# Optimization experiments

Measured on AMD Instinct MI355X. Metric: run time of the kernel, lower is better.

The kernel has to match this reference:

```python
import jax, jax.numpy as jnp
import numpy as np

SHAPE = (4, 16, 16)          # (t, h, w) latent shape
E, H, L = 576, 16, 6         # embd_dim, n_head, n_layer
DK = E // H                  # head dim = 36
SEQ = int(np.prod(SHAPE))    # 1024
B = 2


def _layernorm(x, s, b):
    m = x.mean(-1, keepdims=True)
    v = ((x - m) ** 2).mean(-1, keepdims=True)
    return (x - m) * jax.lax.rsqrt(v + 1e-5) * s + b


def _masks():
    # causal lower-triangular mask and L1 distance-decay mask (FullAttention.__init__)
    causal = np.tril(np.ones((SEQ, SEQ), dtype=bool))
    grids = np.meshgrid(*[np.arange(s) for s in SHAPE], indexing='ij')
    coords = np.stack([g.ravel() for g in grids], -1)          # [SEQ, 3]
    dist = np.abs(coords[:, None, :] - coords[None, :, :]).sum(-1).astype(np.float32)
    dm = np.exp(-dist / dist[0, -1])                            # max distance = dist[0, SEQ-1]
    return jnp.asarray(causal), jnp.asarray(dm)


def setup_inputs() -> dict:
    key = jax.random.key(0)
    ks = jax.random.split(key, 12)
    f32 = jnp.float32
    std = 1.0 / np.sqrt(E)
    pe = E // 3
    d = {}
    d['x'] = jax.random.normal(ks[0], (B, *SHAPE, E), f32)
    d['sos'] = jax.random.normal(ks[1], (E,), f32) * 0.02
    d['pe0'] = jax.random.normal(ks[2], (SHAPE[0], pe), f32) * 0.01
    d['pe1'] = jax.random.normal(ks[3], (SHAPE[1], pe), f32) * 0.01
    d['pe2'] = jax.random.normal(ks[4], (SHAPE[2], pe), f32) * 0.01
    d['ln1_s'] = jnp.ones((L, E), f32); d['ln1_b'] = jnp.zeros((L, E), f32)
    d['wq'] = jax.random.normal(ks[5], (L, E, E), f32) * std
    d['wk'] = jax.random.normal(ks[6], (L, E, E), f32) * std
    d['wv'] = jax.random.normal(ks[7], (L, E, E), f32) * std
    d['wo'] = jax.random.normal(ks[8], (L, E, E), f32) * (1.0 / np.sqrt(E * L))
    d['bo'] = jnp.zeros((L, E), f32)
    d['ln2_s'] = jnp.ones((L, E), f32); d['ln2_b'] = jnp.zeros((L, E), f32)
    d['w1'] = jax.random.normal(ks[9], (L, E, 4 * E), f32) * std
    d['b1'] = jnp.zeros((L, 4 * E), f32)
    d['w2'] = jax.random.normal(ks[10], (L, 4 * E, E), f32) * (1.0 / np.sqrt(4 * E))
    d['b2'] = jnp.zeros((L, E), f32)
    return d


def _forward(x, sos, pe0, pe1, pe2, ln1_s, ln1_b, wq, wk, wv, wo, bo,
             ln2_s, ln2_b, w1, b1, w2, b2):
    b = x.shape[0]
    causal, dm = _masks()
    h = x.reshape(b, SEQ, E)
    # RightShift: prepend learned SOS token, drop last
    h = jnp.concatenate([jnp.broadcast_to(sos, (b, 1, E)), h[:, :-1]], axis=1)
    # AddBroadcastPosEmbed (dim=-1): per-axis embeddings concatenated on channels
    pos = jnp.concatenate([
        jnp.broadcast_to(pe0[:, None, None, :], (*SHAPE, E // 3)),
        jnp.broadcast_to(pe1[None, :, None, :], (*SHAPE, E // 3)),
        jnp.broadcast_to(pe2[None, None, :, :], (*SHAPE, E // 3)),
    ], axis=-1).reshape(SEQ, E)
    h = h + pos
    scale = 1.0 / np.sqrt(DK)
    for l in range(L):  # fixed small layer loop
        y = _layernorm(h, ln1_s[l], ln1_b[l])
        q = (y @ wq[l]).reshape(b, SEQ, H, DK).transpose(0, 2, 1, 3)
        k = (y @ wk[l]).reshape(b, SEQ, H, DK).transpose(0, 2, 1, 3)
        v = (y @ wv[l]).reshape(b, SEQ, H, DK).transpose(0, 2, 1, 3)
        s = jnp.einsum('bhqd,bhkd->bhqk', q, k) * scale
        s = s * dm                              # elementwise distance-decay mask
        s = jnp.where(causal, s, -jnp.inf)       # causal masked_fill
        a = jax.nn.softmax(s, axis=-1)
        o = jnp.einsum('bhqk,bhkd->bhqd', a, v)
        o = o.transpose(0, 2, 1, 3).reshape(b, SEQ, E) @ wo[l] + bo[l]
        h = h + o
        y = _layernorm(h, ln2_s[l], ln2_b[l])
        y1 = y @ w1[l] + b1[l]
        y1 = jax.nn.sigmoid(1.702 * y1) * y1     # GeLU2
        h = h + (y1 @ w2[l] + b2[l])
    return h.reshape(b, *SHAPE, E)


def reference(x, sos, pe0, pe1, pe2, ln1_s, ln1_b, wq, wk, wv, wo, bo,
              ln2_s, ln2_b, w1, b1, w2, b2):
    return _forward(x, sos, pe0, pe1, pe2, ln1_s, ln1_b, wq, wk, wv, wo, bo,
                    ln2_s, ln2_b, w1, b1, w2, b2)
```

## Files before the change

kernel.cpp:

```cpp
#include <hip/hip_runtime.h>


#define E_    576
#define SEQ_  1024
#define B_    2
#define NH_   16
#define DK_   36
#define DKP_  64
#define NL_   6
#define FF_   2304
#define ROWS_ 2048
#define PSTRIDE_ 1179648

typedef unsigned short u16;
typedef unsigned int u32;
typedef float f32x4 __attribute__((ext_vector_type(4)));
typedef float f32x16 __attribute__((ext_vector_type(16)));
typedef __bf16 bf16x8 __attribute__((ext_vector_type(8)));
typedef __bf16 bf16x4 __attribute__((ext_vector_type(4)));

#define MFMA16(a, b, c) __builtin_amdgcn_mfma_f32_16x16x32_bf16((a), (b), (c), 0, 0, 0)
#define MFMA32(a, b, c) __builtin_amdgcn_mfma_f32_32x32x16_bf16((a), (b), (c), 0, 0, 0)

__device__ __forceinline__ float bf2f(u16 u) {
    return __uint_as_float(((unsigned)u) << 16);
}
__device__ __forceinline__ u16 f2bf(float f) {
    unsigned u = __float_as_uint(f);
    u += 0x7fffu + ((u >> 16) & 1u);
    return (u16)(u >> 16);
}
__device__ __forceinline__ float load_in(const void* p, size_t i, int isf32) {
    return isf32 ? ((const float*)p)[i] : bf2f(((const u16*)p)[i]);
}
__device__ __forceinline__ bf16x8 ldg8(const u16* p) {
    uint4 u = *(const uint4*)p;
    bf16x8 r;
    __builtin_memcpy(&r, &u, 16);
    return r;
}
__device__ __forceinline__ void gload_lds16(const u16* g, u16* l) {
    __builtin_amdgcn_global_load_lds(
        (const __attribute__((address_space(1))) unsigned int*)g,
        (__attribute__((address_space(3))) unsigned int*)l, 16, 0, 0);
}

__global__ void detect_kernel(const u16* __restrict__ x, int* __restrict__ flag)
{
    __shared__ float red[4];
    int lane = threadIdx.x & 63, wave = threadIdx.x >> 6;
    float mx = 0.f;
    for (int i = threadIdx.x; i < 4096; i += 256) {
        float v = fabsf(bf2f(x[i]));
        if (v < 3e38f) mx = fmaxf(mx, v);
    }
    for (int off = 1; off < 64; off <<= 1) mx = fmaxf(mx, __shfl_xor(mx, off));
    if (lane == 0) red[wave] = mx;
    __syncthreads();
    if (threadIdx.x == 0) {
        float m = fmaxf(fmaxf(red[0], red[1]), fmaxf(red[2], red[3]));
        *flag = (m > 1e6f) ? 1 : 0;
    }
}

__global__ __launch_bounds__(256) void repack_kernel(
    const void* __restrict__ wq, const void* __restrict__ wk,
    const void* __restrict__ wv, const void* __restrict__ wo,
    const void* __restrict__ w1, const void* __restrict__ w2,
    u16* __restrict__ wT, const int* __restrict__ flagp)
{
    __shared__ u32 tile[64 * 33];
    int isf32 = *flagp;
    int idx = blockIdx.x, l = blockIdx.z;
    const void* src;
    u16* dst;
    size_t sbase;
    int R, C, cx, ry;
    if (idx < 324) {
        int t4 = idx / 81, rem = idx - t4 * 81;
        ry = rem / 9; cx = rem % 9; R = 576; C = 576;
        src = (t4 == 0) ? wq : (t4 == 1) ? wk : (t4 == 2) ? wv : wo;
        sbase = (size_t)l * 331776;
        dst = wT + (size_t)l * 3981312 + t4 * 331776;
    } else if (idx < 648) {
        int rem = idx - 324;
        ry = rem / 36; cx = rem % 36; R = 576; C = 2304;
        src = w1; sbase = (size_t)l * 1327104;
        dst = wT + (size_t)l * 3981312 + 1327104;
    } else {
        int rem = idx - 648;
        ry = rem / 9; cx = rem % 9; R = 2304; C = 576;
        src = w2; sbase = (size_t)l * 1327104;
        dst = wT + (size_t)l * 3981312 + 2654208;
    }
    int r0 = ry * 64, c0 = cx * 64;
    int t = threadIdx.x;
    if (isf32) {
        int chunk = t & 15, row = t >> 4;
        f32x4 vf4[4];
        #pragma unroll
        for (int i = 0; i < 4; i++) {
            int rr = row + i * 16;
            size_t g = sbase + (size_t)(r0 + rr) * C + c0 + chunk * 4;
            vf4[i] = *(const f32x4*)((const float*)src + g);
        }
        #pragma unroll
        for (int i = 0; i < 4; i++) {
            int rr = row + i * 16;
            u32 lo = (u32)f2bf(vf4[i][0]) | ((u32)f2bf(vf4[i][1]) << 16);
            u32 hi = (u32)f2bf(vf4[i][2]) | ((u32)f2bf(vf4[i][3]) << 16);
            tile[rr * 33 + chunk * 2] = lo;
            tile[rr * 33 + chunk * 2 + 1] = hi;
        }
    } else {
        int c8 = t & 7, row = t >> 3;
        uint4 vq[2];
        #pragma unroll
        for (int i = 0; i < 2; i++) {
            int rr = row + i * 32;
            size_t g = sbase + (size_t)(r0 + rr) * C + c0 + c8 * 8;
            vq[i] = *(const uint4*)((const u16*)src + g);
        }
        #pragma unroll
        for (int i = 0; i < 2; i++) {
            int rr = row + i * 32;
            u32* w = &tile[rr * 33 + c8 * 4];
            w[0] = vq[i].x; w[1] = vq[i].y; w[2] = vq[i].z; w[3] = vq[i].w;
        }
    }
    __syncthreads();
    u16* tbase = dst + ((size_t)cx * (R >> 6) + ry) * 4096;
    int k8 = t & 7, nl = t >> 3;
    #pragma unroll
    for (int i = 0; i < 2; i++) {
        int nn = nl + i * 32;
        int hw = nn >> 1, sh = (nn & 1) * 16;
        u32 v[8];
        #pragma unroll
        for (int j = 0; j < 8; j++)
            v[j] = (tile[(8 * k8 + j) * 33 + hw] >> sh) & 0xffffu;
        uint4 o;
        o.x = v[0] | (v[1] << 16);
        o.y = v[2] | (v[3] << 16);
        o.z = v[4] | (v[5] << 16);
        o.w = v[6] | (v[7] << 16);
        ((uint4*)(tbase + nn * 64))[k8 ^ (nn & 7)] = o;
    }
}

__global__ void embed_kernel(
    const void* __restrict__ x, const void* __restrict__ sos,
    const void* __restrict__ pe0, const void* __restrict__ pe1,
    const void* __restrict__ pe2, float* __restrict__ h,
    const int* __restrict__ flagp)
{
    int isf32 = *flagp;
    int row = blockIdx.x;
    int e = threadIdx.x;
    int s = row & 1023;
    float v = (s == 0) ? load_in(sos, e, isf32)
                       : load_in(x, (size_t)(row - 1) * E_ + e, isf32);
    int t = s >> 8, hh = (s >> 4) & 15, ww = s & 15;
    float p = (e < 192) ? load_in(pe0, t * 192 + e, isf32)
            : (e < 384) ? load_in(pe1, hh * 192 + e - 192, isf32)
                        : load_in(pe2, ww * 192 + e - 384, isf32);
    h[(size_t)row * E_ + e] = v + p;
}

template <int NPART>
__global__ __launch_bounds__(256) void ln_kernel(
    float* __restrict__ h, u16* __restrict__ y,
    const float* __restrict__ parts,
    const void* __restrict__ sc, const void* __restrict__ bi,
    int off0, const int* __restrict__ flagp)
{
    int isf32 = *flagp;
    int lane = threadIdx.x & 63, wave = threadIdx.x >> 6;
    int row = blockIdx.x * 4 + wave;
    float* hr = h + (size_t)row * E_;
    float v[9], s = 0.f, sq = 0.f;
    #pragma unroll
    for (int j = 0; j < 9; j++) {
        int e = lane + j * 64;
        float t = hr[e];
        #pragma unroll
        for (int pk = 0; pk < NPART; pk++)
            t += parts[(size_t)pk * PSTRIDE_ + (size_t)row * E_ + e];
        if (NPART > 0) hr[e] = t;
        v[j] = t;
        s += t;
        sq += t * t;
    }
    for (int off = 1; off < 64; off <<= 1) {
        s += __shfl_xor(s, off);
        sq += __shfl_xor(sq, off);
    }
    float mean = s * (1.0f / E_);
    float var = sq * (1.0f / E_) - mean * mean;
    float r = rsqrtf(var + 1e-5f);
    #pragma unroll
    for (int j = 0; j < 9; j++) {
        int e = lane + j * 64;
        float sce = load_in(sc, off0 + e, isf32);
        float bie = load_in(bi, off0 + e, isf32);
        y[(size_t)row * E_ + e] = f2bf((v[j] - mean) * r * sce + bie);
    }
}

template <int MODE, int SPLITK>
__global__ __launch_bounds__(512) void gemm_kernel(
    const u16* __restrict__ A, const u16* __restrict__ BtBase, int K,
    const void* __restrict__ bias, int boff, float* __restrict__ pout,
    u16* __restrict__ out, u16* __restrict__ qb, u16* __restrict__ kb,
    u16* __restrict__ vtb, const int* __restrict__ flagp)
{
    __shared__ u16 lA[8192];
    __shared__ u16 lB[4096];
    int t = threadIdx.x;
    int lane = t & 63, wave = t >> 6;
    int lw = lane & 15, lq = lane >> 4;
    int wx = wave >> 1, wy = wave & 1;
    int m0 = blockIdx.x * 128, n0 = blockIdx.y * 64;
    int z = blockIdx.z / SPLITK, kz = blockIdx.z % SPLITK;
    int Ks = K / SPLITK, kbase = kz * Ks;

    const u16* Bt = BtBase + (MODE == 0 ? (size_t)z * 331776 : 0);
    int rowS = t >> 3;
    int gc = (t & 7) ^ (rowS & 7);
    const u16* gA = A + (size_t)(m0 + rowS) * K + kbase + gc * 8;
    const u16* gB = Bt + ((size_t)(n0 >> 6)) * ((size_t)K << 6)
                  + (size_t)kbase * 64 + (size_t)t * 8;
    size_t rstep = (size_t)64 * K;

    f32x4 acc[2][2];
    for (int mi = 0; mi < 2; mi++)
        for (int ni = 0; ni < 2; ni++)
            for (int r = 0; r < 4; r++) acc[mi][ni][r] = 0.f;

    for (int kc = 0; kc < Ks; kc += 64) {
        gload_lds16(gA + kc,         &lA[t * 8]);
        gload_lds16(gA + rstep + kc, &lA[4096 + t * 8]);
        gload_lds16(gB + kc * 64,    &lB[t * 8]);
        __syncthreads();
        #pragma unroll
        for (int ks = 0; ks < 2; ks++) {
            int csw = ((ks * 4 + lq) ^ (lw & 7)) * 8;
            bf16x8 bf0 = ldg8(&lB[(wy * 32 + lw) * 64 + csw]);
            bf16x8 bf1 = ldg8(&lB[(wy * 32 + 16 + lw) * 64 + csw]);
            #pragma unroll
            for (int mi = 0; mi < 2; mi++) {
                bf16x8 af = ldg8(&lA[(wx * 32 + mi * 16 + lw) * 64 + csw]);
                acc[mi][0] = MFMA16(af, bf0, acc[mi][0]);
                acc[mi][1] = MFMA16(af, bf1, acc[mi][1]);
            }
        }
        __syncthreads();
    }

    int isf32 = (MODE != 0) ? *flagp : 0;
    #pragma unroll
    for (int ni = 0; ni < 2; ni++) {
        int n = n0 + wy * 32 + ni * 16 + lw;
        float bn = 0.f;
        if (MODE == 2 || ((MODE == 1 || MODE == 3) && kz == 0))
            bn = load_in(bias, boff + n, isf32);
        #pragma unroll
        for (int mi = 0; mi < 2; mi++) {
            #pragma unroll
            for (int r = 0; r < 4; r++) {
                int m = m0 + wx * 32 + mi * 16 + lq * 4 + r;
                float v = acc[mi][ni][r];
                if (MODE == 0) {
                    int b = m >> 10, s = m & 1023;
                    int head = n / 36, d = n - head * 36;
                    size_t bh = (size_t)(b * NH_ + head);
                    if (z == 0)
                        qb[(bh * SEQ_ + s) * DKP_ + d] = f2bf(v * (1.0f / 6.0f));
                    else if (z == 1)
                        kb[(bh * SEQ_ + s) * DKP_ + d] = f2bf(v);
                    else
                        vtb[(bh * DKP_ + d) * SEQ_ + s] = f2bf(v);
                } else if (MODE == 2) {
                    float tt = v + bn;
                    out[(size_t)m * FF_ + n] = f2bf(tt / (1.0f + __expf(-1.702f * tt)));
                } else {
                    pout[(size_t)kz * PSTRIDE_ + (size_t)m * E_ + n] = v + bn;
                }
            }
        }
    }
}

__global__ __launch_bounds__(256, 2) void attn_kernel(
    const u16* __restrict__ qb, const u16* __restrict__ kb,
    const u16* __restrict__ vtb, u16* __restrict__ ob)
{
    __shared__ float sm[4][32], sl[4][32], so[4][32][37];
    int lane = threadIdx.x & 63, wave = threadIdx.x >> 6;
    int q5 = lane & 31, hi = lane >> 5, hi8 = hi * 8;
    int L = blockIdx.x;
    int bh = L & 31;
    int qt = 31 - (L >> 5);
    int head = bh & 15, b = bh >> 4;
    int q0 = qt * 32;

    const u16* qrow = qb + ((size_t)bh * SEQ_ + q0 + q5) * DKP_ + hi8;
    bf16x8 qf[4];
    #pragma unroll
    for (int d16 = 0; d16 < 4; d16++) qf[d16] = ldg8(qrow + d16 * 16);

    int tq = q0 >> 8;
    int hq = ((q0 >> 4) & 15) + (q5 >> 4);
    int qg = q0 + q5;
    int wq = q5 & 15;
    float ew8[8];
    #pragma unroll
    for (int j = 0; j < 8; j++)
        ew8[j] = __expf((float)abs(wq - (j + hi8)) * (-1.0f / 33.0f));

    float m_i = -1e30f, l_i = 0.f;
    f32x16 oacc[2];
    #pragma unroll
    for (int Dt = 0; Dt < 2; Dt++)
        #pragma unroll
        for (int r = 0; r < 16; r++) oacc[Dt][r] = 0.f;

    int kp = (q5 & ~12) | ((q5 & 4) << 1) | ((q5 & 8) >> 1);
    const u16* kbh = kb + (size_t)bh * SEQ_ * DKP_;
    const u16* vbh = vtb + (size_t)bh * DKP_ * SEQ_;

    int nch = (qt >> 1) + 1;
    for (int c = wave; c < nch; c += 4) {
        int kv0 = c * 64;
        bf16x8 kf[2][4], vf[2][4];
        #pragma unroll
        for (int T = 0; T < 2; T++) {
            const u16* kr = kbh + (size_t)(kv0 + T * 32 + kp) * DKP_ + hi8;
            #pragma unroll
            for (int d16 = 0; d16 < 4; d16++) kf[T][d16] = ldg8(kr + d16 * 16);
        }
        #pragma unroll
        for (int s = 0; s < 4; s++)
            vf[0][s] = ldg8(vbh + (size_t)q5 * SEQ_ + kv0 + s * 16 + hi8);
        f32x16 st[2];
        #pragma unroll
        for (int T = 0; T < 2; T++) {
            f32x16 tt;
            #pragma unroll
            for (int r = 0; r < 16; r++) tt[r] = 0.f;
            #pragma unroll
            for (int d16 = 0; d16 < 4; d16++)
                tt = MFMA32(kf[T][d16], qf[d16], tt);
            st[T] = tt;
        }
        #pragma unroll
        for (int s = 0; s < 4; s++)
            vf[1][s] = ldg8(vbh + (size_t)(32 + q5) * SEQ_ + kv0 + s * 16 + hi8);
        int tk = kv0 >> 8, hk0 = (kv0 >> 4) & 15;
        float sB[4];
        #pragma unroll
        for (int i = 0; i < 4; i++)
            sB[i] = __expf((float)(abs(tq - tk) + abs(hq - hk0 - i))
                           * (-1.0f / 33.0f));
        float vv[2][16];
        #pragma unroll
        for (int T = 0; T < 2; T++)
            #pragma unroll
            for (int r = 0; r < 16; r++) {
                int j = (r & 3) + ((r >> 2) & 1) * 4;
                int hidx = T * 2 + ((r >> 3) & 1);
                vv[T][r] = st[T][r] * (sB[hidx] * ew8[j]);
            }
        if (c == nch - 1) {
            #pragma unroll
            for (int T = 0; T < 2; T++)
                #pragma unroll
                for (int r = 0; r < 16; r++) {
                    int key = kv0 + T * 32 + ((r >> 3) & 1) * 16 + hi8
                            + (r & 3) + ((r >> 2) & 1) * 4;
                    if (key > qg) vv[T][r] = -1e30f;
                }
        }
        float mloc = -1e30f;
        #pragma unroll
        for (int T = 0; T < 2; T++)
            #pragma unroll
            for (int r = 0; r < 16; r++) mloc = fmaxf(mloc, vv[T][r]);
        mloc = fmaxf(mloc, __shfl_xor(mloc, 32));
        float mn = fmaxf(m_i, mloc);
        float alpha = __expf(m_i - mn);
        m_i = mn;
        float p[2][16];
        float rs = 0.f;
        #pragma unroll
        for (int T = 0; T < 2; T++)
            #pragma unroll
            for (int r = 0; r < 16; r++) {
                p[T][r] = __expf(vv[T][r] - mn);
                rs += p[T][r];
            }
        rs += __shfl_xor(rs, 32);
        l_i = l_i * alpha + rs;
        #pragma unroll
        for (int Dt = 0; Dt < 2; Dt++)
            #pragma unroll
            for (int r = 0; r < 16; r++) oacc[Dt][r] *= alpha;
        bf16x8 pf[4];
        #pragma unroll
        for (int T = 0; T < 2; T++)
            #pragma unroll
            for (int sp = 0; sp < 2; sp++)
                #pragma unroll
                for (int e = 0; e < 8; e++)
                    pf[T * 2 + sp][e] = (__bf16)p[T][sp * 8 + e];
        #pragma unroll
        for (int Dt = 0; Dt < 2; Dt++)
            #pragma unroll
            for (int s = 0; s < 4; s++)
                oacc[Dt] = MFMA32(vf[Dt][s], pf[s], oacc[Dt]);
    }

    if (hi == 0) { sm[wave][q5] = m_i; sl[wave][q5] = l_i; }
    #pragma unroll
    for (int r = 0; r < 16; r++)
        so[wave][q5][(r & 3) + 8 * (r >> 2) + 4 * hi] = oacc[0][r];
    if (hi == 0) {
        #pragma unroll
        for (int r = 0; r < 4; r++)
            so[wave][q5][32 + r] = oacc[1][r];
    }
    __syncthreads();
    for (int i = threadIdx.x; i < 32 * DK_; i += 256) {
        int row = i / DK_, col = i - row * DK_;
        float M = fmaxf(fmaxf(sm[0][row], sm[1][row]),
                        fmaxf(sm[2][row], sm[3][row]));
        float Lm = 0.f, O = 0.f;
        #pragma unroll
        for (int w = 0; w < 4; w++) {
            float f = __expf(sm[w][row] - M);
            Lm += f * sl[w][row];
            O += f * so[w][row][col];
        }
        ob[((size_t)b * SEQ_ + q0 + row) * E_ + head * DK_ + col] = f2bf(O / Lm);
    }
}

__global__ void out_kernel(const float* __restrict__ h,
                           const float* __restrict__ p3,
                           void* __restrict__ out,
                           const int* __restrict__ flagp)
{
    int isf32 = *flagp;
    size_t i = (size_t)blockIdx.x * blockDim.x + threadIdx.x;
    float v = h[i] + p3[i] + p3[i + PSTRIDE_] + p3[i + 2 * PSTRIDE_]
            + p3[i + 3 * PSTRIDE_];
    if (isf32) ((float*)out)[i] = v;
    else       ((u16*)out)[i] = f2bf(v);
}

extern "C" void kernel_launch(void* const* d_in, const int* in_sizes, int n_in,
                              void* d_out, int out_size, void* d_ws,
                              size_t ws_size, hipStream_t stream)
{
    const void* x    = d_in[0];
    const void* sos  = d_in[1];
    const void* pe0  = d_in[2];
    const void* pe1  = d_in[3];
    const void* pe2  = d_in[4];
    const void* ln1s = d_in[5];
    const void* ln1b = d_in[6];
    const void* wq   = d_in[7];
    const void* wk   = d_in[8];
    const void* wv   = d_in[9];
    const void* wo   = d_in[10];
    const void* bo   = d_in[11];
    const void* ln2s = d_in[12];
    const void* ln2b = d_in[13];
    const void* w1   = d_in[14];
    const void* b1   = d_in[15];
    const void* w2   = d_in[16];
    const void* b2   = d_in[17];

    char* ws = (char*)d_ws;
    u16*   qbuf  = (u16*)(ws + 0);
    u16*   kbuf  = (u16*)(ws + 4194304);
    u16*   vtbuf = (u16*)(ws + 8388608);
    float* h     = (float*)(ws + 12582912);
    u16*   y     = (u16*)(ws + 17301504);
    u16*   o     = (u16*)(ws + 19660800);
    u16*   y1    = (u16*)(ws + 22020096);
    u16*   wT    = (u16*)(ws + 31457280);
    int*   flag  = (int*)(ws + 79233024);
    float* p1    = (float*)(ws + 83886080);
    float* p3    = (float*)(ws + 100663296);

    hipMemsetAsync(ws, 0, 12582912, stream);
    detect_kernel<<<1, 256, 0, stream>>>((const u16*)x, flag);
    repack_kernel<<<dim3(972, 1, 6), 256, 0, stream>>>(
        wq, wk, wv, wo, w1, w2, wT, flag);
    embed_kernel<<<ROWS_, E_, 0, stream>>>(x, sos, pe0, pe1, pe2, h, flag);

    for (int l = 0; l < NL_; l++) {
        u16* wTl = wT + (size_t)l * 3981312;
        if (l == 0)
            ln_kernel<0><<<512, 256, 0, stream>>>(h, y, nullptr, ln1s, ln1b,
                                                  l * E_, flag);
        else
            ln_kernel<4><<<512, 256, 0, stream>>>(h, y, p3, ln1s, ln1b,
                                                  l * E_, flag);
        gemm_kernel<0, 1><<<dim3(16, 9, 3), 512, 0, stream>>>(
            y, wTl, E_, nullptr, 0, nullptr, nullptr, qbuf, kbuf, vtbuf, flag);
        attn_kernel<<<dim3(1024), 256, 0, stream>>>(qbuf, kbuf, vtbuf, o);
        gemm_kernel<1, 3><<<dim3(16, 9, 3), 512, 0, stream>>>(
            o, wTl + 995328, E_, bo, l * E_, p1, nullptr, nullptr, nullptr, nullptr, flag);
        ln_kernel<3><<<512, 256, 0, stream>>>(h, y, p1, ln2s, ln2b,
                                              l * E_, flag);
        gemm_kernel<2, 1><<<dim3(16, 36, 1), 512, 0, stream>>>(
            y, wTl + 1327104, E_, b1, l * FF_, nullptr, y1, nullptr, nullptr, nullptr, flag);
        gemm_kernel<3, 4><<<dim3(16, 9, 4), 512, 0, stream>>>(
            y1, wTl + 2654208, FF_, b2, l * E_, p3, nullptr, nullptr, nullptr, nullptr, flag);
    }
    out_kernel<<<4608, 256, 0, stream>>>(h, p3, d_out, flag);
}
```

Measured before the change: 701.1 us.

## Double-buffer GEMM LDS tiles and halve block size to 64x64

The GEMM kernel now keeps two LDS buffers for the A and B tiles and issues the global-to-LDS loads for the next K chunk before computing the current one. A single waitcnt-plus-barrier per iteration replaces the two __syncthreads. Block tiles shrink from 128x64 with 512 threads to 64x64 with 256 threads, which doubles the grid along M to give more blocks for latency hiding. The cost is more total global loads of B per output and extra LDS per block.

```diff
diff --git a/kernel.cpp b/kernel.cpp
--- a/kernel.cpp
+++ b/kernel.cpp
@@ -21,6 +21,8 @@
 
 #define MFMA16(a, b, c) __builtin_amdgcn_mfma_f32_16x16x32_bf16((a), (b), (c), 0, 0, 0)
 #define MFMA32(a, b, c) __builtin_amdgcn_mfma_f32_32x32x16_bf16((a), (b), (c), 0, 0, 0)
+
+#define VMBAR() asm volatile("s_waitcnt vmcnt(0)\n\ts_barrier" ::: "memory")
 
 __device__ __forceinline__ float bf2f(u16 u) {
     return __uint_as_float(((unsigned)u) << 16);
@@ -208,19 +210,19 @@
 }
 
 template <int MODE, int SPLITK>
-__global__ __launch_bounds__(512) void gemm_kernel(
+__global__ __launch_bounds__(256) void gemm_kernel(
     const u16* __restrict__ A, const u16* __restrict__ BtBase, int K,
     const void* __restrict__ bias, int boff, float* __restrict__ pout,
     u16* __restrict__ out, u16* __restrict__ qb, u16* __restrict__ kb,
     u16* __restrict__ vtb, const int* __restrict__ flagp)
 {
-    __shared__ u16 lA[8192];
-    __shared__ u16 lB[4096];
+    __shared__ u16 lA[2][4096];
+    __shared__ u16 lB[2][4096];
     int t = threadIdx.x;
     int lane = t & 63, wave = t >> 6;
     int lw = lane & 15, lq = lane >> 4;
     int wx = wave >> 1, wy = wave & 1;
-    int m0 = blockIdx.x * 128, n0 = blockIdx.y * 64;
+    int m0 = blockIdx.x * 64, n0 = blockIdx.y * 64;
     int z = blockIdx.z / SPLITK, kz = blockIdx.z % SPLITK;
     int Ks = K / SPLITK, kbase = kz * Ks;
 
@@ -228,34 +230,46 @@
     int rowS = t >> 3;
     int gc = (t & 7) ^ (rowS & 7);
     const u16* gA = A + (size_t)(m0 + rowS) * K + kbase + gc * 8;
+    size_t rstep = (size_t)32 * K;
     const u16* gB = Bt + ((size_t)(n0 >> 6)) * ((size_t)K << 6)
                   + (size_t)kbase * 64 + (size_t)t * 8;
-    size_t rstep = (size_t)64 * K;
 
     f32x4 acc[2][2];
     for (int mi = 0; mi < 2; mi++)
         for (int ni = 0; ni < 2; ni++)
             for (int r = 0; r < 4; r++) acc[mi][ni][r] = 0.f;
 
-    for (int kc = 0; kc < Ks; kc += 64) {
-        gload_lds16(gA + kc,         &lA[t * 8]);
-        gload_lds16(gA + rstep + kc, &lA[4096 + t * 8]);
-        gload_lds16(gB + kc * 64,    &lB[t * 8]);
-        __syncthreads();
+    auto stage = [&](int buf, int kc) {
+        gload_lds16(gA + kc,          &lA[buf][t * 8]);
+        gload_lds16(gA + rstep + kc,  &lA[buf][2048 + t * 8]);
+        gload_lds16(gB + kc * 64,        &lB[buf][t * 8]);
+        gload_lds16(gB + kc * 64 + 2048, &lB[buf][2048 + t * 8]);
+    };
+    auto compute = [&](int buf) {
         #pragma unroll
         for (int ks = 0; ks < 2; ks++) {
             int csw = ((ks * 4 + lq) ^ (lw & 7)) * 8;
-            bf16x8 bf0 = ldg8(&lB[(wy * 32 + lw) * 64 + csw]);
-            bf16x8 bf1 = ldg8(&lB[(wy * 32 + 16 + lw) * 64 + csw]);
+            bf16x8 bf0 = ldg8(&lB[buf][(wy * 32 + lw) * 64 + csw]);
+            bf16x8 bf1 = ldg8(&lB[buf][(wy * 32 + 16 + lw) * 64 + csw]);
             #pragma unroll
             for (int mi = 0; mi < 2; mi++) {
-                bf16x8 af = ldg8(&lA[(wx * 32 + mi * 16 + lw) * 64 + csw]);
+                bf16x8 af = ldg8(&lA[buf][(wx * 32 + mi * 16 + lw) * 64 + csw]);
                 acc[mi][0] = MFMA16(af, bf0, acc[mi][0]);
                 acc[mi][1] = MFMA16(af, bf1, acc[mi][1]);
             }
         }
-        __syncthreads();
-    }
+    };
+
+    stage(0, 0);
+    VMBAR();
+    int cur = 0;
+    for (int kc = 0; kc + 64 < Ks; kc += 64) {
+        stage(cur ^ 1, kc + 64);
+        compute(cur);
+        VMBAR();
+        cur ^= 1;
+    }
+    compute(cur);
 
     int isf32 = (MODE != 0) ? *flagp : 0;
     #pragma unroll
@@ -508,16 +522,16 @@
         else
             ln_kernel<4><<<512, 256, 0, stream>>>(h, y, p3, ln1s, ln1b,
                                                   l * E_, flag);
-        gemm_kernel<0, 1><<<dim3(16, 9, 3), 512, 0, stream>>>(
+        gemm_kernel<0, 1><<<dim3(32, 9, 3), 256, 0, stream>>>(
             y, wTl, E_, nullptr, 0, nullptr, nullptr, qbuf, kbuf, vtbuf, flag);
         attn_kernel<<<dim3(1024), 256, 0, stream>>>(qbuf, kbuf, vtbuf, o);
-        gemm_kernel<1, 3><<<dim3(16, 9, 3), 512, 0, stream>>>(
+        gemm_kernel<1, 3><<<dim3(32, 9, 3), 256, 0, stream>>>(
             o, wTl + 995328, E_, bo, l * E_, p1, nullptr, nullptr, nullptr, nullptr, flag);
         ln_kernel<3><<<512, 256, 0, stream>>>(h, y, p1, ln2s, ln2b,
                                               l * E_, flag);
-        gemm_kernel<2, 1><<<dim3(16, 36, 1), 512, 0, stream>>>(
+        gemm_kernel<2, 1><<<dim3(32, 36, 1), 256, 0, stream>>>(
             y, wTl + 1327104, E_, b1, l * FF_, nullptr, y1, nullptr, nullptr, nullptr, flag);
-        gemm_kernel<3, 4><<<dim3(16, 9, 4), 512, 0, stream>>>(
+        gemm_kernel<3, 4><<<dim3(32, 9, 4), 256, 0, stream>>>(
             y1, wTl + 2654208, FF_, b2, l * E_, p3, nullptr, nullptr, nullptr, nullptr, flag);
     }
     out_kernel<<<4608, 256, 0, stream>>>(h, p3, d_out, flag);
```

Result: slower. 728.2 us (+3.9%).
